# Kernel tuning notes

Hardware: AMD Instinct MI355X
Metric: run time of the kernel (lower is better)

The kernel has to match this reference:

```python
import jax, jax.numpy as jnp
import numpy as np

MAX_RES = 5.0  # max_residue_magnitude
DG = 16       # deform_groups
KH = KW = 3
K = KH * KW
PAD = 1
STRIDE = 1
DIL = 1


def conv3x3(x, w, b):
    y = jax.lax.conv_general_dilated(
        x, w, window_strides=(1, 1), padding='SAME',
        dimension_numbers=('NCHW', 'OIHW', 'NCHW'))
    return y + b[None, :, None, None]


def lrelu(x):
    return jnp.where(x >= 0, x, 0.1 * x)


def deform_conv2d(x, offset, mask, weight, bias):
    # x: [B,C,H,W]; offset: [B,2*DG*K,Ho,Wo]; mask: [B,DG*K,Ho,Wo]
    B, C, H, W = x.shape
    Cout = weight.shape[0]
    Ho = (H + 2 * PAD - DIL * (KH - 1) - 1) // STRIDE + 1
    Wo = (W + 2 * PAD - DIL * (KW - 1) - 1) // STRIDE + 1
    Cg = C // DG

    # torchvision layout: offset channel = g*(2*K) + 2*k + {0:y, 1:x}
    off = offset.reshape(B, DG, K, 2, Ho, Wo)
    oy, ox = off[:, :, :, 0], off[:, :, :, 1]           # [B,DG,K,Ho,Wo]
    msk = mask.reshape(B, DG, K, Ho, Wo)

    ki = DIL * (jnp.arange(K) // KW)                    # [K] kernel row offsets
    kj = DIL * (jnp.arange(K) % KW)
    base_y = STRIDE * jnp.arange(Ho) - PAD              # [Ho]
    base_x = STRIDE * jnp.arange(Wo) - PAD              # [Wo]
    py = base_y[None, None, None, :, None] + ki[None, None, :, None, None] + oy
    px = base_x[None, None, None, None, :] + kj[None, None, :, None, None] + ox

    xg = x.reshape(B, DG, Cg, H * W)

    y0 = jnp.floor(py)
    x0 = jnp.floor(px)
    wy1 = py - y0
    wx1 = px - x0

    def corner(iy, ix, w_c):
        valid = ((iy >= 0) & (iy <= H - 1) & (ix >= 0) & (ix <= W - 1)).astype(x.dtype)
        iyc = jnp.clip(iy, 0, H - 1).astype(jnp.int32)
        ixc = jnp.clip(ix, 0, W - 1).astype(jnp.int32)
        idx = (iyc * W + ixc).reshape(B, DG, 1, K * Ho * Wo)
        g = jnp.take_along_axis(
            xg, jnp.broadcast_to(idx, (B, DG, Cg, K * Ho * Wo)), axis=3)
        g = g.reshape(B, DG, Cg, K, Ho, Wo)
        return g * (w_c * valid)[:, :, None]

    val = (corner(y0, x0, (1 - wy1) * (1 - wx1))
           + corner(y0, x0 + 1, (1 - wy1) * wx1)
           + corner(y0 + 1, x0, wy1 * (1 - wx1))
           + corner(y0 + 1, x0 + 1, wy1 * wx1))

    val = val * msk[:, :, None]                          # modulation
    val = val.reshape(B, C, K, Ho, Wo)                   # columns
    out = jnp.einsum('bckhw,ock->bohw', val, weight.reshape(Cout, C, K))
    return out + bias[None, :, None, None]


def setup_inputs() -> dict:
    key = jax.random.key(0)
    ks = jax.random.split(key, 12)
    B, H, W = 1, 192, 192
    inp = {
        'x':    jax.random.normal(ks[0], (B, 128, H, W), jnp.float32),
        'cond': jax.random.normal(ks[1], (B, 192, H, W), jnp.float32),
        'weight': jax.random.normal(ks[2], (64, 128, 3, 3), jnp.float32) * 0.03,
        'bias':   jax.random.normal(ks[3], (64,), jnp.float32) * 0.01,
        'w1': jax.random.normal(ks[4], (64, 192, 3, 3), jnp.float32) * 0.03,
        'b1': jax.random.normal(ks[5], (64,), jnp.float32) * 0.01,
        'w2': jax.random.normal(ks[6], (64, 64, 3, 3), jnp.float32) * 0.05,
        'b2': jax.random.normal(ks[7], (64,), jnp.float32) * 0.01,
        'w3': jax.random.normal(ks[8], (64, 64, 3, 3), jnp.float32) * 0.05,
        'b3': jax.random.normal(ks[9], (64,), jnp.float32) * 0.01,
        'w4': jax.random.normal(ks[10], (432, 64, 3, 3), jnp.float32) * 0.05,
        'b4': jax.random.normal(ks[11], (432,), jnp.float32) * 0.01,
    }
    return inp


def reference(x, cond, weight, bias, w1, b1, w2, b2, w3, b3, w4, b4):
    h = lrelu(conv3x3(cond, w1, b1))
    h = lrelu(conv3x3(h, w2, b2))
    h = lrelu(conv3x3(h, w3, b3))
    out = conv3x3(h, w4, b4)                       # [B, 27*DG, H, W]
    offset, mask = out[:, :18 * DG], out[:, 18 * DG:]
    offset = MAX_RES * jnp.tanh(offset)
    mask = jax.nn.sigmoid(mask)
    return deform_conv2d(x, offset, mask, weight, bias)
```

## Files before the change

### kernel.cpp

```cpp
#include <hip/hip_runtime.h>
#include <hip/hip_bf16.h>
#include <math.h>

#define IMG_H 192
#define IMG_W 192
#define NPIX (IMG_H * IMG_W)
#define PADW 194
#define PPIX (PADW * PADW)
#define PH 208
#define PW 208

typedef _Float16 h8 __attribute__((ext_vector_type(8)));
typedef _Float16 h4 __attribute__((ext_vector_type(4)));
typedef float f32x4 __attribute__((ext_vector_type(4)));

__device__ __forceinline__ float act_tanh5(float x) {
    const float t = __expf(2.f * x);
    return 5.f * (t - 1.f) / (t + 1.f);
}
__device__ __forceinline__ float act_sig(float x) {
    return 1.f / (1.f + __expf(-x));
}

typedef __attribute__((address_space(1))) const unsigned int GU32;
typedef __attribute__((address_space(3))) unsigned int LU32;
__device__ __forceinline__ void cp16(const void* g, void* l) {
    __builtin_amdgcn_global_load_lds((GU32*)g, (LU32*)l, 16, 0, 0);
}

__global__ __launch_bounds__(256) void cond_pack_k(
    const float* __restrict__ src, _Float16* __restrict__ dst)
{
    const int y = blockIdx.x;
    const int c = blockIdx.y;
    const int x = threadIdx.x;
    if (x >= PADW) return;
    const bool inb = (y >= 1 && y <= IMG_H && x >= 1 && x <= IMG_W);
    h8 v[4];
#pragma unroll
    for (int j = 0; j < 32; j++)
        ((_Float16*)v)[j] = inb
            ? (_Float16)src[(size_t)(c * 32 + j) * NPIX + (y - 1) * IMG_W + (x - 1)]
            : (_Float16)0.f;
    h8* d = (h8*)&dst[((size_t)c * PPIX + (size_t)y * PADW + x) * 32];
    d[0] = v[0]; d[1] = v[1]; d[2] = v[2]; d[3] = v[3];
}

template<int CIN, int COP, int COUT>
__device__ __forceinline__ void pack_body(
    int bx, const float* __restrict__ src, _Float16* __restrict__ dst)
{
    const int chunk = bx / 9, k = bx % 9;
    for (int i = threadIdx.x; i < COP * 32; i += 256) {
        const int co = i >> 5, cil = i & 31;
        float v = 0.f;
        if (co < COUT)
            v = src[((size_t)(co * CIN + chunk * 32 + cil)) * 9 + k];
        dst[(size_t)bx * COP * 32 + i] = (_Float16)v;
    }
}

__global__ __launch_bounds__(256) void pack_all_w_k(
    const float* __restrict__ w1, const float* __restrict__ w2,
    const float* __restrict__ w3, const float* __restrict__ w4,
    _Float16* __restrict__ wp1, _Float16* __restrict__ wp2,
    _Float16* __restrict__ wp3, _Float16* __restrict__ wp4)
{
    const int b = blockIdx.x;
    if      (b < 54) pack_body<192, 64, 64>(b, w1, wp1);
    else if (b < 72) pack_body<64, 64, 64>(b - 54, w2, wp2);
    else if (b < 90) pack_body<64, 64, 64>(b - 72, w3, wp3);
    else             pack_body<64, 448, 432>(b - 90, w4, wp4);
}

__global__ __launch_bounds__(192) void xg_pack_k(
    const float* __restrict__ x, _Float16* __restrict__ xg)
{
    const int y  = blockIdx.x;
    const int dg = blockIdx.y;
    const int xc = threadIdx.x;
    h8 v;
#pragma unroll
    for (int chl = 0; chl < 8; chl++)
        v[chl] = (_Float16)x[(size_t)(dg * 8 + chl) * NPIX + y * IMG_W + xc];
    *(h8*)&xg[(((size_t)dg * PH + y + 6) * PW + xc + 6) * 8] = v;
}

__global__ __launch_bounds__(256) void wdg_pack_k(
    const float* __restrict__ w, _Float16* __restrict__ wdg)
{
    const int i = blockIdx.x * 256 + threadIdx.x;
    if (i >= 16 * 64 * 96) return;
    const int ks = i % 96;
    const int rest = i / 96;
    const int co = rest % 64;
    const int dg = rest / 64;
    const int k = ks >> 3, chl = ks & 7;
    float v = 0.f;
    if (ks < 72)
        v = w[((size_t)co * 128 + dg * 8 + chl) * 9 + k];
    wdg[i] = (_Float16)v;
}

template<int CHUNKS, int ACT, int COP, int T8>
__global__ __launch_bounds__(256) void conv_lds_k(
    const _Float16* __restrict__ in,
    const _Float16* __restrict__ wpk,
    const float* __restrict__ bias,
    _Float16* __restrict__ out)
{
    constexpr int HALO = T8 ? 10 : 18;
    constexpr int NF   = T8 ? 1 : 4;
    constexpr int TDIM = T8 ? 24 : 12;
    constexpr int TSZ  = T8 ? 8 : 16;
    constexpr int INU  = HALO * HALO * 4;
    constexpr int ROWU = HALO * 4;

    __shared__ _Float16 in_lds[HALO * HALO * 32];
    __shared__ _Float16 w_lds[9 * 64 * 32];

    const int t    = threadIdx.x;
    const int lane = t & 63;
    const int wv   = __builtin_amdgcn_readfirstlane(t >> 6);
    const int col  = lane & 15;
    const int quad = lane >> 4;
    const int bx   = blockIdx.x;
    const int tx0  = (bx % TDIM) * TSZ;
    const int ty0  = (bx / TDIM) * TSZ;
    const int cobase = blockIdx.y * 64;

    f32x4 acc[4][NF];
#pragma unroll
    for (int m = 0; m < 4; m++)
#pragma unroll
        for (int s = 0; s < NF; s++) {
            f32x4 z = {0.f, 0.f, 0.f, 0.f};
            acc[m][s] = z;
        }

    for (int c = 0; c < CHUNKS; c++) {
        __syncthreads();
        {
            const char* gbase = (const char*)in + (size_t)c * PPIX * 64;
            char* lbase = (char*)in_lds + (size_t)wv * 64 * 16;
#pragma unroll
            for (int i = 0; i < (INU + 255) / 256; i++) {
                const int j = t + i * 256;
                if (j < INU) {
                    const int row = j / ROWU;
                    const int u   = j - row * ROWU;
                    cp16(gbase + ((size_t)(ty0 + row) * PADW + tx0) * 64 + u * 16,
                         lbase + (size_t)i * 256 * 16);
                }
            }
        }
        {
            const char* gw = (const char*)wpk
                + ((size_t)(c * 9) * COP + cobase) * 64 + t * 16;
            char* lw = (char*)w_lds + (size_t)wv * 64 * 16;
#pragma unroll
            for (int k = 0; k < 9; k++)
                cp16(gw + (size_t)k * COP * 64, lw + k * 4096);
        }
        __syncthreads();

#pragma unroll
        for (int k = 0; k < 9; k++) {
            const int ky = k / 3, kx = k % 3;
            h8 af[4];
#pragma unroll
            for (int m = 0; m < 4; m++)
                af[m] = *(const h8*)&w_lds[(k * 64 + m * 16 + col) * 32 + quad * 8];
            h8 bf[NF];
            if (T8) {
                bf[0] = *(const h8*)&in_lds[
                    ((2 * wv + (col >> 3) + ky) * HALO + (col & 7) + kx) * 32 + quad * 8];
            } else {
#pragma unroll
                for (int s = 0; s < NF; s++)
                    bf[s] = *(const h8*)&in_lds[
                        ((4 * wv + s + ky) * HALO + col + kx) * 32 + quad * 8];
            }
#pragma unroll
            for (int m = 0; m < 4; m++)
#pragma unroll
                for (int s = 0; s < NF; s++)
                    acc[m][s] = __builtin_amdgcn_mfma_f32_16x16x32_f16(
                        af[m], bf[s], acc[m][s], 0, 0, 0);
        }
    }

#pragma unroll
    for (int m = 0; m < 4; m++) {
#pragma unroll
        for (int s = 0; s < NF; s++) {
            int gy, gx;
            if (T8) { gy = ty0 + 2 * wv + (col >> 3); gx = tx0 + (col & 7); }
            else    { gy = ty0 + 4 * wv + s;          gx = tx0 + col; }
            const int ca = cobase + m * 16 + quad * 4;
            if (ACT == 1) {
                h4 st;
#pragma unroll
                for (int r = 0; r < 4; r++) {
                    float v = acc[m][s][r] + bias[ca + r];
                    st[r] = (_Float16)((v >= 0.f) ? v : 0.1f * v);
                }
                *(h4*)&out[((size_t)(ca >> 5) * PPIX + (size_t)(gy + 1) * PADW + (gx + 1)) * 32
                           + (ca & 31)] = st;
            } else {
#pragma unroll
                for (int r = 0; r < 4; r++) {
                    const int co = ca + r;
                    if (co < 432) {
                        const int pix = gy * IMG_W + gx;
                        out[((size_t)(pix >> 5) * 432 + co) * 32 + (pix & 31)] =
                            (_Float16)(acc[m][s][r] + bias[co]);
                    }
                }
            }
        }
    }
}

__global__ __launch_bounds__(256) void deform_mfma_k(
    const _Float16* __restrict__ xg,
    const _Float16* __restrict__ od,
    const _Float16* __restrict__ wdg,
    const float* __restrict__ bias,
    float* __restrict__ out)
{
    __shared__ __align__(16) _Float16 val4[4][32][104];

    const int t    = threadIdx.x;
    const int lane = t & 63;
    const int wv   = __builtin_amdgcn_readfirstlane(t >> 6);
    const int col  = lane & 15;
    const int quad = lane >> 4;
    const int bxr  = blockIdx.x;
    const int bx   = (bxr & 7) * 144 + (bxr >> 3);
    const int gy   = bx / 6;
    const int gx0  = (bx % 6) * 32;

    const _Float16* odseg = od + (size_t)bx * 432 * 32;

    for (int i = t; i < 4 * 32 * 4; i += 256) {
        const int dgl = i >> 7;
        const int r   = i & 127;
        const int px  = r >> 2;
        const int j   = r & 3;
        h8 z = {0, 0, 0, 0, 0, 0, 0, 0};
        *(h8*)&val4[dgl][px][72 + 8 * j] = z;
    }

    f32x4 acc[2];
    {
        f32x4 z = {0.f, 0.f, 0.f, 0.f};
        acc[0] = z; acc[1] = z;
    }

    for (int dq = 0; dq < 4; dq++) {
        __syncthreads();

        for (int idx = t; idx < 1152; idx += 256) {
            const int pxl  = idx & 31;
            const int rest = idx >> 5;
            const int k    = rest % 9;
            const int dgl  = rest / 9;
            const int dg   = dq * 4 + dgl;
            const int rr   = dgl * 9 + k;
            const float oy = act_tanh5((float)odseg[(dq * 72 + 2 * rr) * 32 + pxl]);
            const float ox = act_tanh5((float)odseg[(dq * 72 + 2 * rr + 1) * 32 + pxl]);
            const float m  = act_sig((float)odseg[(288 + dq * 36 + rr) * 32 + pxl]);
            const float py  = (float)(gy - 1 + k / 3) + oy;
            const float pxx = (float)(gx0 + pxl - 1 + k % 3) + ox;
            const float y0 = floorf(py), x0 = floorf(pxx);
            const float fy = py - y0, fx = pxx - x0;
            const int iy = (int)y0 + 6, ix = (int)x0 + 6;
            const _Float16* p = xg + (((size_t)dg * PH + iy) * PW + ix) * 8;
            const h8 c00 = *(const h8*)p;
            const h8 c01 = *(const h8*)(p + 8);
            const h8 c10 = *(const h8*)(p + PW * 8);
            const h8 c11 = *(const h8*)(p + PW * 8 + 8);
            const float ey = 1.f - fy, ex = 1.f - fx;
            const _Float16 s00 = (_Float16)(ey * ex * m);
            const _Float16 s01 = (_Float16)(ey * fx * m);
            const _Float16 s10 = (_Float16)(fy * ex * m);
            const _Float16 s11 = (_Float16)(fy * fx * m);
            const h8 v = c00 * s00 + c01 * s01 + c10 * s10 + c11 * s11;
            *(h8*)&val4[dgl][pxl][k * 8] = v;
        }
        __syncthreads();

#pragma unroll
        for (int dgl = 0; dgl < 4; dgl++) {
            const int dg = dq * 4 + dgl;
            const _Float16* wbase = wdg + ((size_t)dg * 64 + wv * 16 + col) * 96;
#pragma unroll
            for (int ks = 0; ks < 3; ks++) {
                const h8 a  = *(const h8*)(wbase + ks * 32 + quad * 8);
                const h8 b0 = *(const h8*)&val4[dgl][col][ks * 32 + quad * 8];
                const h8 b1 = *(const h8*)&val4[dgl][16 + col][ks * 32 + quad * 8];
                acc[0] = __builtin_amdgcn_mfma_f32_16x16x32_f16(a, b0, acc[0], 0, 0, 0);
                acc[1] = __builtin_amdgcn_mfma_f32_16x16x32_f16(a, b1, acc[1], 0, 0, 0);
            }
        }
    }

    const int co = wv * 16 + quad * 4;
#pragma unroll
    for (int n = 0; n < 2; n++) {
        const int gx = gx0 + n * 16 + col;
#pragma unroll
        for (int r = 0; r < 4; r++)
            out[(size_t)(co + r) * NPIX + gy * IMG_W + gx] = acc[n][r] + bias[co + r];
    }
}

extern "C" void kernel_launch(void* const* d_in, const int* in_sizes, int n_in,
                              void* d_out, int out_size, void* d_ws, size_t ws_size,
                              hipStream_t stream) {
    (void)in_sizes; (void)n_in; (void)out_size; (void)ws_size;

    const float* x      = (const float*)d_in[0];
    const float* cond   = (const float*)d_in[1];
    const float* weight = (const float*)d_in[2];
    const float* bias   = (const float*)d_in[3];
    const float* w1     = (const float*)d_in[4];
    const float* b1     = (const float*)d_in[5];
    const float* w2     = (const float*)d_in[6];
    const float* b2     = (const float*)d_in[7];
    const float* w3     = (const float*)d_in[8];
    const float* b3     = (const float*)d_in[9];
    const float* w4     = (const float*)d_in[10];
    const float* b4     = (const float*)d_in[11];
    float* out = (float*)d_out;

    char* ws = (char*)d_ws;
    size_t off = 0;
    auto take = [&](size_t bytes) -> char* {
        char* p = ws + off;
        off = (off + bytes + 255) & ~(size_t)255;
        return p;
    };
    _Float16* act_cond = (_Float16*)take((size_t)6 * PPIX * 32 * 2);
    _Float16* pb_all   = (_Float16*)take((size_t)3 * 2 * PPIX * 32 * 2);
    _Float16* pb1 = pb_all;
    _Float16* pb2 = pb1 + (size_t)2 * PPIX * 32;
    _Float16* pb3 = pb2 + (size_t)2 * PPIX * 32;
    _Float16* od  = (_Float16*)take((size_t)432 * NPIX * 2);
    _Float16* wp1 = (_Float16*)take((size_t)54 * 64 * 32 * 2);
    _Float16* wp2 = (_Float16*)take((size_t)18 * 64 * 32 * 2);
    _Float16* wp3 = (_Float16*)take((size_t)18 * 64 * 32 * 2);
    _Float16* wp4 = (_Float16*)take((size_t)18 * 448 * 32 * 2);
    _Float16* xg  = (_Float16*)take((size_t)16 * PH * PW * 8 * 2);
    _Float16* wdg = (_Float16*)take((size_t)16 * 64 * 96 * 2);

    hipMemsetAsync(pb_all, 0, (size_t)3 * 2 * PPIX * 32 * 2, stream);
    hipMemsetAsync(xg,     0, (size_t)16 * PH * PW * 8 * 2, stream);

    hipLaunchKernelGGL(cond_pack_k, dim3(PADW, 6), dim3(256), 0, stream, cond, act_cond);
    hipLaunchKernelGGL(pack_all_w_k, dim3(108), dim3(256), 0, stream,
                       w1, w2, w3, w4, wp1, wp2, wp3, wp4);
    hipLaunchKernelGGL(xg_pack_k,  dim3(192, 16), dim3(192), 0, stream, x, xg);
    hipLaunchKernelGGL(wdg_pack_k, dim3((16 * 64 * 96 + 255) / 256), dim3(256), 0, stream, weight, wdg);

    hipLaunchKernelGGL((conv_lds_k<6, 1, 64, 1>),  dim3(576, 1), dim3(256), 0, stream, act_cond, wp1, b1, pb1);
    hipLaunchKernelGGL((conv_lds_k<2, 1, 64, 1>),  dim3(576, 1), dim3(256), 0, stream, pb1, wp2, b2, pb2);
    hipLaunchKernelGGL((conv_lds_k<2, 1, 64, 1>),  dim3(576, 1), dim3(256), 0, stream, pb2, wp3, b3, pb3);
    hipLaunchKernelGGL((conv_lds_k<2, 2, 448, 0>), dim3(144, 7), dim3(256), 0, stream, pb3, wp4, b4, od);
    hipLaunchKernelGGL(deform_mfma_k, dim3(1152), dim3(256), 0, stream, xg, od, wdg, bias, out);
}
```

Measured before the change: 260.5 us.

## Fuse prep kernels into one launch and zero only padding borders

Merges the cond, x, conv-weight and deform-weight packing kernels into a single block-partitioned prep kernel, removing several launches. The two full-buffer hipMemsetAsync calls are replaced by writing zeros only to the halo and border regions of the padded activation buffers. This avoids tens of MB of memset traffic, but relies on later conv kernels always writing the full interior of those buffers.

New measurement: 240.6 us. -7.6%, faster.

```diff
diff --git a/kernel.cpp b/kernel.cpp
--- a/kernel.cpp
+++ b/kernel.cpp
@@ -26,24 +26,6 @@
 typedef __attribute__((address_space(3))) unsigned int LU32;
 __device__ __forceinline__ void cp16(const void* g, void* l) {
     __builtin_amdgcn_global_load_lds((GU32*)g, (LU32*)l, 16, 0, 0);
-}
-
-__global__ __launch_bounds__(256) void cond_pack_k(
-    const float* __restrict__ src, _Float16* __restrict__ dst)
-{
-    const int y = blockIdx.x;
-    const int c = blockIdx.y;
-    const int x = threadIdx.x;
-    if (x >= PADW) return;
-    const bool inb = (y >= 1 && y <= IMG_H && x >= 1 && x <= IMG_W);
-    h8 v[4];
-#pragma unroll
-    for (int j = 0; j < 32; j++)
-        ((_Float16*)v)[j] = inb
-            ? (_Float16)src[(size_t)(c * 32 + j) * NPIX + (y - 1) * IMG_W + (x - 1)]
-            : (_Float16)0.f;
-    h8* d = (h8*)&dst[((size_t)c * PPIX + (size_t)y * PADW + x) * 32];
-    d[0] = v[0]; d[1] = v[1]; d[2] = v[2]; d[3] = v[3];
 }
 
 template<int CIN, int COP, int COUT>
@@ -60,46 +42,109 @@
     }
 }
 
-__global__ __launch_bounds__(256) void pack_all_w_k(
-    const float* __restrict__ w1, const float* __restrict__ w2,
-    const float* __restrict__ w3, const float* __restrict__ w4,
-    _Float16* __restrict__ wp1, _Float16* __restrict__ wp2,
-    _Float16* __restrict__ wp3, _Float16* __restrict__ wp4)
+__global__ __launch_bounds__(256) void prep_all_k(
+    const float* __restrict__ cond, const float* __restrict__ w1,
+    const float* __restrict__ w2, const float* __restrict__ w3,
+    const float* __restrict__ w4, const float* __restrict__ x,
+    const float* __restrict__ weight,
+    _Float16* __restrict__ act_cond, _Float16* __restrict__ wp1,
+    _Float16* __restrict__ wp2, _Float16* __restrict__ wp3,
+    _Float16* __restrict__ wp4, _Float16* __restrict__ xg,
+    _Float16* __restrict__ wdg, _Float16* __restrict__ pb_all)
 {
-    const int b = blockIdx.x;
-    if      (b < 54) pack_body<192, 64, 64>(b, w1, wp1);
-    else if (b < 72) pack_body<64, 64, 64>(b - 54, w2, wp2);
-    else if (b < 90) pack_body<64, 64, 64>(b - 72, w3, wp3);
-    else             pack_body<64, 448, 432>(b - 90, w4, wp4);
-}
-
-__global__ __launch_bounds__(192) void xg_pack_k(
-    const float* __restrict__ x, _Float16* __restrict__ xg)
-{
-    const int y  = blockIdx.x;
-    const int dg = blockIdx.y;
-    const int xc = threadIdx.x;
-    h8 v;
-#pragma unroll
-    for (int chl = 0; chl < 8; chl++)
-        v[chl] = (_Float16)x[(size_t)(dg * 8 + chl) * NPIX + y * IMG_W + xc];
-    *(h8*)&xg[(((size_t)dg * PH + y + 6) * PW + xc + 6) * 8] = v;
-}
-
-__global__ __launch_bounds__(256) void wdg_pack_k(
-    const float* __restrict__ w, _Float16* __restrict__ wdg)
-{
-    const int i = blockIdx.x * 256 + threadIdx.x;
-    if (i >= 16 * 64 * 96) return;
-    const int ks = i % 96;
-    const int rest = i / 96;
-    const int co = rest % 64;
-    const int dg = rest / 64;
-    const int k = ks >> 3, chl = ks & 7;
-    float v = 0.f;
-    if (ks < 72)
-        v = w[((size_t)co * 128 + dg * 8 + chl) * 9 + k];
-    wdg[i] = (_Float16)v;
+    int b = blockIdx.x;
+    const int t = threadIdx.x;
+
+    if (b < 1164) {
+        const int y = b % 194;
+        const int c = b / 194;
+        if (t >= PADW) return;
+        const bool inb = (y >= 1 && y <= IMG_H && t >= 1 && t <= IMG_W);
+        h8 v[4];
+#pragma unroll
+        for (int j = 0; j < 32; j++)
+            ((_Float16*)v)[j] = inb
+                ? (_Float16)cond[(size_t)(c * 32 + j) * NPIX + (y - 1) * IMG_W + (t - 1)]
+                : (_Float16)0.f;
+        h8* d = (h8*)&act_cond[((size_t)c * PPIX + (size_t)y * PADW + t) * 32];
+        d[0] = v[0]; d[1] = v[1]; d[2] = v[2]; d[3] = v[3];
+        return;
+    }
+    b -= 1164;
+
+    if (b < 3072) {
+        const int y  = b % 192;
+        const int dg = b / 192;
+        if (t < 192) {
+            h8 v;
+#pragma unroll
+            for (int chl = 0; chl < 8; chl++)
+                v[chl] = (_Float16)x[(size_t)(dg * 8 + chl) * NPIX + y * IMG_W + t];
+            *(h8*)&xg[(((size_t)dg * PH + y + 6) * PW + t + 6) * 8] = v;
+        }
+        return;
+    }
+    b -= 3072;
+
+    if (b < 108) {
+        if      (b < 54) pack_body<192, 64, 64>(b, w1, wp1);
+        else if (b < 72) pack_body<64, 64, 64>(b - 54, w2, wp2);
+        else if (b < 90) pack_body<64, 64, 64>(b - 72, w3, wp3);
+        else             pack_body<64, 448, 432>(b - 90, w4, wp4);
+        return;
+    }
+    b -= 108;
+
+    if (b < 384) {
+        const int i = b * 256 + t;
+        if (i < 16 * 64 * 96) {
+            const int ks = i % 96;
+            const int rest = i / 96;
+            const int co = rest % 64;
+            const int dg = rest / 64;
+            const int k = ks >> 3, chl = ks & 7;
+            float v = 0.f;
+            if (ks < 72)
+                v = weight[((size_t)co * 128 + dg * 8 + chl) * 9 + k];
+            wdg[i] = (_Float16)v;
+        }
+        return;
+    }
+    b -= 384;
+
+    if (b < 400) {
+        const int idx = b * 256 + t;
+        if (idx < 16 * 6400) {
+            const int dg = idx / 6400;
+            int r = idx % 6400;
+            int row, col;
+            if (r < 1248)      { row = r / 208;              col = r % 208; }
+            else if (r < 3328) { r -= 1248; row = 198 + r / 208; col = r % 208; }
+            else if (r < 4480) { r -= 3328; row = 6 + r / 6;     col = r % 6; }
+            else               { r -= 4480; row = 6 + r / 10;    col = 198 + r % 10; }
+            h8 z = {0, 0, 0, 0, 0, 0, 0, 0};
+            *(h8*)&xg[(((size_t)dg * PH + row) * PW + col) * 8] = z;
+        }
+        return;
+    }
+    b -= 400;
+
+    {
+        const int idx = b * 256 + t;
+        if (idx < 6 * 772 * 4) {
+            const int px_id = idx >> 2, part = idx & 3;
+            const int plane = px_id / 772;
+            int r = px_id % 772;
+            int y, xx;
+            if (r < 194)      { y = 0;            xx = r; }
+            else if (r < 388) { y = 193;          xx = r - 194; }
+            else if (r < 580) { y = 1 + (r - 388); xx = 0; }
+            else              { y = 1 + (r - 580); xx = 193; }
+            h8 z = {0, 0, 0, 0, 0, 0, 0, 0};
+            *(h8*)&pb_all[((size_t)plane * PPIX + (size_t)y * PADW + xx) * 32 + part * 8] = z;
+        }
+        return;
+    }
 }
 
 template<int CHUNKS, int ACT, int COP, int T8>
@@ -355,14 +400,9 @@
     _Float16* xg  = (_Float16*)take((size_t)16 * PH * PW * 8 * 2);
     _Float16* wdg = (_Float16*)take((size_t)16 * 64 * 96 * 2);
 
-    hipMemsetAsync(pb_all, 0, (size_t)3 * 2 * PPIX * 32 * 2, stream);
-    hipMemsetAsync(xg,     0, (size_t)16 * PH * PW * 8 * 2, stream);
-
-    hipLaunchKernelGGL(cond_pack_k, dim3(PADW, 6), dim3(256), 0, stream, cond, act_cond);
-    hipLaunchKernelGGL(pack_all_w_k, dim3(108), dim3(256), 0, stream,
-                       w1, w2, w3, w4, wp1, wp2, wp3, wp4);
-    hipLaunchKernelGGL(xg_pack_k,  dim3(192, 16), dim3(192), 0, stream, x, xg);
-    hipLaunchKernelGGL(wdg_pack_k, dim3((16 * 64 * 96 + 255) / 256), dim3(256), 0, stream, weight, wdg);
+    hipLaunchKernelGGL(prep_all_k, dim3(5201), dim3(256), 0, stream,
+                       cond, w1, w2, w3, w4, x, weight,
+                       act_cond, wp1, wp2, wp3, wp4, xg, wdg, pb_all);
 
     hipLaunchKernelGGL((conv_lds_k<6, 1, 64, 1>),  dim3(576, 1), dim3(256), 0, stream, act_cond, wp1, b1, pb1);
     hipLaunchKernelGGL((conv_lds_k<2, 1, 64, 1>),  dim3(576, 1), dim3(256), 0, stream, pb1, wp2, b2, pb2);
```
